# Optimization experiments

Hardware: AMD Instinct MI355X
Metric: run time of the kernel (lower is better)

## Reference

```python
import jax, jax.numpy as jnp
import numpy as np

D_MODEL = 1024
N_HEADS = 16
D_HEAD = D_MODEL // N_HEADS


def setup_inputs() -> dict:
    key = jax.random.key(0)
    ks = jax.random.split(key, 11)
    B, L = 2, 2048
    s = 1.0 / np.sqrt(D_MODEL)
    return {
        "query": jax.random.normal(ks[0], (B, L, D_MODEL), jnp.float32),
        "key": jax.random.normal(ks[1], (B, L, D_MODEL), jnp.float32),
        "value": jax.random.normal(ks[2], (B, L, D_MODEL), jnp.float32),
        "Wq": jax.random.normal(ks[3], (D_MODEL, D_MODEL), jnp.float32) * s,
        "bq": jnp.zeros((D_MODEL,), jnp.float32),
        "Wk": jax.random.normal(ks[4], (D_MODEL, D_MODEL), jnp.float32) * s,
        "bk": jnp.zeros((D_MODEL,), jnp.float32),
        "Wv": jax.random.normal(ks[5], (D_MODEL, D_MODEL), jnp.float32) * s,
        "bv": jnp.zeros((D_MODEL,), jnp.float32),
        "Wo": jax.random.normal(ks[6], (D_MODEL, D_MODEL), jnp.float32) * s,
        "bo": jnp.zeros((D_MODEL,), jnp.float32),
    }


def reference(query, key, value, Wq, bq, Wk, bk, Wv, bv, Wo, bo):
    B, Lq, _ = query.shape
    Lk = key.shape[1]
    scale = D_HEAD ** -0.5
    # projections; weights stored as [in, out] (torch Linear applies x @ W.T; here W is already transposed)
    q = (query @ Wq + bq).reshape(B, Lq, N_HEADS, D_HEAD).transpose(0, 2, 1, 3)  # [B,H,Lq,dh]
    k = (key @ Wk + bk).reshape(B, Lk, N_HEADS, D_HEAD).transpose(0, 2, 1, 3)
    v = (value @ Wv + bv).reshape(B, Lk, N_HEADS, D_HEAD).transpose(0, 2, 1, 3)
    scores = jnp.einsum('bhqd,bhkd->bhqk', q, k) * scale  # [B,H,Lq,Lk]
    # causal mask (is_causal=True)
    causal = jnp.triu(jnp.ones((Lq, Lk), dtype=bool), k=1)
    scores = jnp.where(causal, -jnp.inf, scores)
    attn = jax.nn.softmax(scores, axis=-1)
    out = jnp.einsum('bhqk,bhkd->bhqd', attn, v)  # [B,H,Lq,dh]
    out = out.transpose(0, 2, 1, 3).reshape(B, Lq, D_MODEL)
    return out @ Wo + bo
```

## Files before the change

kernel.cpp:

```cpp
#include <hip/hip_runtime.h>
#include <hip/hip_bf16.h>

typedef __bf16 bf16x8 __attribute__((ext_vector_type(8)));
typedef __bf16 bf16x4 __attribute__((ext_vector_type(4)));
typedef float floatx4 __attribute__((ext_vector_type(4)));

#define MFMA16(a, b, c) __builtin_amdgcn_mfma_f32_16x16x32_bf16(a, b, c, 0, 0, 0)
#define AS1 __attribute__((address_space(1)))
#define AS3 __attribute__((address_space(3)))

constexpr int D = 1024;
constexpr int L = 2048;
constexpr int BB = 2;
constexpr int DH = 64;
constexpr float NEG_BIG = -1e30f;
constexpr float SCALE_LOG2E = 0.125f * 1.4426950408889634f;

__device__ __forceinline__ void gld16(const __bf16* g, __bf16* l) {
  __builtin_amdgcn_global_load_lds((AS1 void*)g, (AS3 void*)l, 16, 0, 0);
}

__global__ __launch_bounds__(256) void cvt_x(const float* __restrict__ xq, const float* __restrict__ xk,
                                             const float* __restrict__ xv, __bf16* __restrict__ out) {
  const int z = blockIdx.z;
  const float* src = z == 0 ? xq : z == 1 ? xk : xv;
  __bf16* dst = out + (size_t)z * BB * L * D;
  const int N = BB * L * D;
  const int stride = gridDim.x * 256 * 4;
  for (int i = (blockIdx.x * 256 + threadIdx.x) * 4; i < N; i += stride) {
    float4 f = *(const float4*)&src[i];
    bf16x4 b = {(__bf16)f.x, (__bf16)f.y, (__bf16)f.z, (__bf16)f.w};
    *(bf16x4*)&dst[i] = b;
  }
}

__global__ void transpose_w(const float* __restrict__ w0, const float* __restrict__ w1,
                            const float* __restrict__ w2, const float* __restrict__ w3,
                            __bf16* __restrict__ out) {
  __shared__ __bf16 tile[32][33];
  int mat = blockIdx.z;
  const float* src = mat == 0 ? w0 : mat == 1 ? w1 : mat == 2 ? w2 : w3;
  __bf16* dst = out + (size_t)mat * D * D;
  int bx = blockIdx.x * 32, by = blockIdx.y * 32;
  int tx = threadIdx.x, ty = threadIdx.y;
#pragma unroll
  for (int i = 0; i < 32; i += 8)
    tile[ty + i][tx] = (__bf16)src[(size_t)(by + ty + i) * D + bx + tx];
  __syncthreads();
#pragma unroll
  for (int i = 0; i < 32; i += 8)
    dst[(size_t)(bx + ty + i) * D + by + tx] = tile[tx][ty + i];
}

__device__ __forceinline__ void gemm_core(const __bf16* __restrict__ A, const __bf16* __restrict__ Bt,
                                          __bf16* sA, __bf16* sB, int m0, int n0,
                                          int wm, int wn, int l15, int quad, int t,
                                          floatx4 (&acc)[4][4]) {
  const int lr = t >> 2;
  const int lc = (t & 3) * 8;
  for (int kb = 0; kb < 1024; kb += 32) {
    gld16(&A[(size_t)(m0 + lr) * 1024 + kb + lc],       &sA[lr * 32 + lc]);
    gld16(&A[(size_t)(m0 + 64 + lr) * 1024 + kb + lc],  &sA[(64 + lr) * 32 + lc]);
    gld16(&Bt[(size_t)(n0 + lr) * 1024 + kb + lc],      &sB[lr * 32 + lc]);
    gld16(&Bt[(size_t)(n0 + 64 + lr) * 1024 + kb + lc], &sB[(64 + lr) * 32 + lc]);
    __syncthreads();

    bf16x8 af[4], bf_[4];
#pragma unroll
    for (int i = 0; i < 4; i++)
      af[i] = *(const bf16x8*)&sA[(wm * 64 + i * 16 + l15) * 32 + quad * 8];
#pragma unroll
    for (int j = 0; j < 4; j++)
      bf_[j] = *(const bf16x8*)&sB[(wn * 64 + j * 16 + l15) * 32 + quad * 8];
#pragma unroll
    for (int i = 0; i < 4; i++)
#pragma unroll
      for (int j = 0; j < 4; j++)
        acc[i][j] = MFMA16(af[i], bf_[j], acc[i][j]);
    __syncthreads();
  }
}

__global__ __launch_bounds__(256) void gemm_proj(const __bf16* __restrict__ xc, const __bf16* __restrict__ wt,
                                                 const float* __restrict__ bq, const float* __restrict__ bk,
                                                 const float* __restrict__ bv, __bf16* __restrict__ qkv) {
  __shared__ __align__(16) __bf16 sA[128 * 32];
  __shared__ __align__(16) __bf16 sB[128 * 32];
  const int z = blockIdx.z;
  const __bf16* A = xc + (size_t)z * BB * L * D;
  const __bf16* Bt = wt + (size_t)z * D * D;
  const float* bias = z == 0 ? bq : z == 1 ? bk : bv;
  __bf16* dst = qkv + (size_t)z * BB * L * D;

  const int t = threadIdx.x;
  const int lane = t & 63;
  const int w = t >> 6;
  const int wm = w >> 1, wn = w & 1;
  const int l15 = lane & 15, quad = lane >> 4;
  const int m0 = blockIdx.y * 128, n0 = blockIdx.x * 128;

  floatx4 acc[4][4];
#pragma unroll
  for (int i = 0; i < 4; i++)
#pragma unroll
    for (int j = 0; j < 4; j++) acc[i][j] = (floatx4){0.f, 0.f, 0.f, 0.f};

  gemm_core(A, Bt, sA, sB, m0, n0, wm, wn, l15, quad, t, acc);

  float bvv[4];
#pragma unroll
  for (int j = 0; j < 4; j++) bvv[j] = bias[n0 + wn * 64 + j * 16 + l15];

#pragma unroll
  for (int i = 0; i < 4; i++) {
    const int rowb = m0 + wm * 64 + i * 16 + quad * 4;
#pragma unroll
    for (int j = 0; j < 4; j++) {
      const int col = n0 + wn * 64 + j * 16 + l15;
      const int h = col >> 6, d = col & 63;
#pragma unroll
      for (int rr = 0; rr < 4; rr++) {
        float val = acc[i][j][rr] + bvv[j];
        const int row = rowb + rr;
        const int b = row >> 11, l = row & 2047;
        if (z == 0) {
          val *= SCALE_LOG2E;
          dst[((size_t)(b * 16 + h) * 2048 + l) * 64 + d] = (__bf16)val;
        } else if (z == 1) {
          dst[((size_t)(b * 16 + h) * 2048 + l) * 64 + d] = (__bf16)val;
        } else {
          dst[((size_t)(b * 16 + h) * 64 + d) * 2048 + l] = (__bf16)val;
        }
      }
    }
  }
}

__global__ __launch_bounds__(256) void gemm_o(const __bf16* __restrict__ ctx, const __bf16* __restrict__ wto,
                                              const float* __restrict__ bo, float* __restrict__ out) {
  __shared__ __align__(16) __bf16 sA[128 * 32];
  __shared__ __align__(16) __bf16 sB[128 * 32];
  const int t = threadIdx.x;
  const int lane = t & 63;
  const int w = t >> 6;
  const int wm = w >> 1, wn = w & 1;
  const int l15 = lane & 15, quad = lane >> 4;
  const int m0 = blockIdx.y * 128, n0 = blockIdx.x * 128;

  floatx4 acc[4][4];
#pragma unroll
  for (int i = 0; i < 4; i++)
#pragma unroll
    for (int j = 0; j < 4; j++) acc[i][j] = (floatx4){0.f, 0.f, 0.f, 0.f};

  gemm_core(ctx, wto, sA, sB, m0, n0, wm, wn, l15, quad, t, acc);

  float bvv[4];
#pragma unroll
  for (int j = 0; j < 4; j++) bvv[j] = bo[n0 + wn * 64 + j * 16 + l15];

#pragma unroll
  for (int i = 0; i < 4; i++) {
    const int rowb = m0 + wm * 64 + i * 16 + quad * 4;
#pragma unroll
    for (int j = 0; j < 4; j++) {
      const int col = n0 + wn * 64 + j * 16 + l15;
#pragma unroll
      for (int rr = 0; rr < 4; rr++)
        out[(size_t)(rowb + rr) * 1024 + col] = acc[i][j][rr] + bvv[j];
    }
  }
}

__global__ __launch_bounds__(256, 4) void flash_attn(const __bf16* __restrict__ q, const __bf16* __restrict__ k,
                                                     const __bf16* __restrict__ vT, __bf16* __restrict__ ctx) {
  __shared__ __align__(16) __bf16 kbuf[2][4096];
  __shared__ __align__(16) __bf16 vbuf[2][4096];

  const int t = threadIdx.x;
  const int lane = t & 63;
  const int w = t >> 6;
  const int l15 = lane & 15, quad = lane >> 4;
  const int bh = blockIdx.y;
  const int qt = (blockIdx.x + blockIdx.y) & 31;
  const int q0 = qt * 64;

  const __bf16* qb = q + (size_t)bh * L * DH;
  const __bf16* kb_ = k + (size_t)bh * L * DH;
  const __bf16* vb = vT + (size_t)bh * DH * L;

  const int qg = q0 + w * 16;
  const int qrow = qg + l15;
  bf16x8 aq0 = *(const bf16x8*)&qb[(size_t)qrow * 64 + quad * 8];
  bf16x8 aq1 = *(const bf16x8*)&qb[(size_t)qrow * 64 + 32 + quad * 8];

  const int c0 = t, c1 = 256 + t;
  const int kr0 = c0 >> 3, kd0 = ((c0 & 7) ^ (kr0 & 7)) * 8;
  const int kr1 = c1 >> 3, kd1 = ((c1 & 7) ^ (kr1 & 7)) * 8;

  floatx4 o[4];
#pragma unroll
  for (int nt = 0; nt < 4; nt++) o[nt] = (floatx4){0.f, 0.f, 0.f, 0.f};
  float psum = 0.f;

  {
    gld16(&kb_[(size_t)kr0 * 64 + kd0], &kbuf[0][c0 * 8]);
    gld16(&kb_[(size_t)kr1 * 64 + kd1], &kbuf[0][c1 * 8]);
    gld16(&vb[(size_t)kr0 * L + kd0],   &vbuf[0][c0 * 8]);
    gld16(&vb[(size_t)kr1 * L + kd1],   &vbuf[0][c1 * 8]);
  }
  __syncthreads();

  for (int it = 0; it <= qt; ++it) {
    const int cur = it & 1;
    const int kt = it * 64;

    if (it < qt) {
      const int ktn = kt + 64;
      gld16(&kb_[(size_t)(ktn + kr0) * 64 + kd0], &kbuf[cur ^ 1][c0 * 8]);
      gld16(&kb_[(size_t)(ktn + kr1) * 64 + kd1], &kbuf[cur ^ 1][c1 * 8]);
      gld16(&vb[(size_t)kr0 * L + ktn + kd0],     &vbuf[cur ^ 1][c0 * 8]);
      gld16(&vb[(size_t)kr1 * L + ktn + kd1],     &vbuf[cur ^ 1][c1 * 8]);
    }

    const bool diag = (it == qt);

#pragma unroll
    for (int sp = 0; sp < 2; ++sp) {
      floatx4 z[2];
#pragma unroll
      for (int u = 0; u < 2; ++u) {
        const int kr = (2 * sp + u) * 16 + l15;
        bf16x8 kf0 = *(const bf16x8*)&kbuf[cur][(kr * 8 + (quad ^ (kr & 7))) * 8];
        bf16x8 kf1 = *(const bf16x8*)&kbuf[cur][(kr * 8 + ((quad + 4) ^ (kr & 7))) * 8];
        floatx4 zz = (floatx4){0.f, 0.f, 0.f, 0.f};
        zz = MFMA16(kf0, aq0, zz);
        zz = MFMA16(kf1, aq1, zz);
        z[u] = zz;
      }

      if (diag) {
#pragma unroll
        for (int u = 0; u < 2; ++u) {
          const int kgb = kt + (2 * sp + u) * 16 + quad * 4;
#pragma unroll
          for (int rr = 0; rr < 4; rr++)
            if (kgb + rr > qrow) z[u][rr] = NEG_BIG;
        }
      }

      bf16x8 pa;
#pragma unroll
      for (int u = 0; u < 2; ++u)
#pragma unroll
        for (int rr = 0; rr < 4; rr++) {
          const float p = __builtin_amdgcn_exp2f(z[u][rr]);
          psum += p;
          pa[u * 4 + rr] = (__bf16)p;
        }

#pragma unroll
      for (int nt = 0; nt < 4; nt++) {
        const int d = nt * 16 + l15;
        const int x0 = (sp * 4 + (quad >> 1)) ^ (d & 7);
        const int x1 = (sp * 4 + 2 + (quad >> 1)) ^ (d & 7);
        union { bf16x8 v8; bf16x4 v4[2]; } uv;
        uv.v4[0] = *(const bf16x4*)&vbuf[cur][(d * 8 + x0) * 8 + (quad & 1) * 4];
        uv.v4[1] = *(const bf16x4*)&vbuf[cur][(d * 8 + x1) * 8 + (quad & 1) * 4];
        o[nt] = MFMA16(pa, uv.v8, o[nt]);
      }
    }
    __syncthreads();
  }

  psum += __shfl_xor(psum, 16);
  psum += __shfl_xor(psum, 32);
  const float invs = 1.f / psum;

  const int b = bh >> 4, h = bh & 15;
#pragma unroll
  for (int rr = 0; rr < 4; rr++) {
    const float inv = __shfl(invs, (lane & 48) + quad * 4 + rr);
    const int row = qg + quad * 4 + rr;
#pragma unroll
    for (int nt = 0; nt < 4; nt++) {
      const int col = h * 64 + nt * 16 + l15;
      ctx[((size_t)b * L + row) * 1024 + col] = (__bf16)(o[nt][rr] * inv);
    }
  }
}

extern "C" void kernel_launch(void* const* d_in, const int* in_sizes, int n_in,
                              void* d_out, int out_size, void* d_ws, size_t ws_size,
                              hipStream_t stream) {
  const float* x_q = (const float*)d_in[0];
  const float* x_k = (const float*)d_in[1];
  const float* x_v = (const float*)d_in[2];
  const float* Wq  = (const float*)d_in[3];
  const float* bq  = (const float*)d_in[4];
  const float* Wk  = (const float*)d_in[5];
  const float* bk  = (const float*)d_in[6];
  const float* Wv  = (const float*)d_in[7];
  const float* bv  = (const float*)d_in[8];
  const float* Wo  = (const float*)d_in[9];
  const float* bo  = (const float*)d_in[10];

  char* ws = (char*)d_ws;
  __bf16* xc  = (__bf16*)ws;
  __bf16* wt  = (__bf16*)(ws + ((size_t)24 << 20));
  __bf16* qkv = (__bf16*)(ws + ((size_t)32 << 20));
  __bf16* ctx = (__bf16*)ws;
  __bf16* qp  = qkv;
  __bf16* kp  = qkv + (size_t)BB * L * D;
  __bf16* vtp = qkv + (size_t)2 * BB * L * D;

  cvt_x<<<dim3(1024, 1, 3), 256, 0, stream>>>(x_q, x_k, x_v, xc);
  transpose_w<<<dim3(32, 32, 4), dim3(32, 8), 0, stream>>>(Wq, Wk, Wv, Wo, wt);
  gemm_proj<<<dim3(8, 32, 3), 256, 0, stream>>>(xc, wt, bq, bk, bv, qkv);
  flash_attn<<<dim3(32, 32), 256, 0, stream>>>(qp, kp, vtp, ctx);
  gemm_o<<<dim3(8, 32), 256, 0, stream>>>(ctx, wt + (size_t)3 * D * D, bo, (float*)d_out);
}
```

Before: 231.2 us.

## Double-buffer LDS tiles in GEMMs and remap block order for XCD locality

The projection and output GEMMs now ping-pong between two LDS buffers, issuing the async global-to-LDS loads for the next K slice before computing on the current one. This removes one barrier per iteration and lets load latency overlap with the MFMAs, at the cost of doubling shared memory per block. Block indices are also remapped so consecutive blocks dispatched round-robin across the 8 XCDs land on neighbouring tiles, which is meant to improve L2 reuse of A and B panels.

```diff
diff --git a/kernel.cpp b/kernel.cpp
--- a/kernel.cpp
+++ b/kernel.cpp
@@ -52,41 +52,60 @@
     dst[(size_t)(bx + ty + i) * D + by + tx] = tile[tx][ty + i];
 }
 
+__device__ __forceinline__ void stage_tile(const __bf16* __restrict__ A, const __bf16* __restrict__ Bt,
+                                           __bf16* sA, __bf16* sB, int m0, int n0, int kb,
+                                           int lr, int lc) {
+  gld16(&A[(size_t)(m0 + lr) * 1024 + kb + lc],       &sA[lr * 32 + lc]);
+  gld16(&A[(size_t)(m0 + 64 + lr) * 1024 + kb + lc],  &sA[(64 + lr) * 32 + lc]);
+  gld16(&Bt[(size_t)(n0 + lr) * 1024 + kb + lc],      &sB[lr * 32 + lc]);
+  gld16(&Bt[(size_t)(n0 + 64 + lr) * 1024 + kb + lc], &sB[(64 + lr) * 32 + lc]);
+}
+
 __device__ __forceinline__ void gemm_core(const __bf16* __restrict__ A, const __bf16* __restrict__ Bt,
-                                          __bf16* sA, __bf16* sB, int m0, int n0,
-                                          int wm, int wn, int l15, int quad, int t,
+                                          __bf16 (&sA)[2][128 * 32], __bf16 (&sB)[2][128 * 32],
+                                          int m0, int n0, int wm, int wn, int l15, int quad, int t,
                                           floatx4 (&acc)[4][4]) {
   const int lr = t >> 2;
   const int lc = (t & 3) * 8;
+
+  stage_tile(A, Bt, sA[0], sB[0], m0, n0, 0, lr, lc);
+  __syncthreads();
+
+  int cur = 0;
   for (int kb = 0; kb < 1024; kb += 32) {
-    gld16(&A[(size_t)(m0 + lr) * 1024 + kb + lc],       &sA[lr * 32 + lc]);
-    gld16(&A[(size_t)(m0 + 64 + lr) * 1024 + kb + lc],  &sA[(64 + lr) * 32 + lc]);
-    gld16(&Bt[(size_t)(n0 + lr) * 1024 + kb + lc],      &sB[lr * 32 + lc]);
-    gld16(&Bt[(size_t)(n0 + 64 + lr) * 1024 + kb + lc], &sB[(64 + lr) * 32 + lc]);
-    __syncthreads();
+    if (kb < 1024 - 32)
+      stage_tile(A, Bt, sA[cur ^ 1], sB[cur ^ 1], m0, n0, kb + 32, lr, lc);
 
     bf16x8 af[4], bf_[4];
 #pragma unroll
     for (int i = 0; i < 4; i++)
-      af[i] = *(const bf16x8*)&sA[(wm * 64 + i * 16 + l15) * 32 + quad * 8];
+      af[i] = *(const bf16x8*)&sA[cur][(wm * 64 + i * 16 + l15) * 32 + quad * 8];
 #pragma unroll
     for (int j = 0; j < 4; j++)
-      bf_[j] = *(const bf16x8*)&sB[(wn * 64 + j * 16 + l15) * 32 + quad * 8];
+      bf_[j] = *(const bf16x8*)&sB[cur][(wn * 64 + j * 16 + l15) * 32 + quad * 8];
 #pragma unroll
     for (int i = 0; i < 4; i++)
 #pragma unroll
       for (int j = 0; j < 4; j++)
         acc[i][j] = MFMA16(af[i], bf_[j], acc[i][j]);
+
     __syncthreads();
+    cur ^= 1;
   }
 }
 
 __global__ __launch_bounds__(256) void gemm_proj(const __bf16* __restrict__ xc, const __bf16* __restrict__ wt,
                                                  const float* __restrict__ bq, const float* __restrict__ bk,
                                                  const float* __restrict__ bv, __bf16* __restrict__ qkv) {
-  __shared__ __align__(16) __bf16 sA[128 * 32];
-  __shared__ __align__(16) __bf16 sB[128 * 32];
-  const int z = blockIdx.z;
+  __shared__ __align__(16) __bf16 sA[2][128 * 32];
+  __shared__ __align__(16) __bf16 sB[2][128 * 32];
+
+  const int flat = (blockIdx.z * 32 + blockIdx.y) * 8 + blockIdx.x;
+  const int s = (flat & 7) * 96 + (flat >> 3);
+  const int z = s >> 8;
+  const int rem = s & 255;
+  const int by = rem >> 3, bx = rem & 7;
+
   const __bf16* A = xc + (size_t)z * BB * L * D;
   const __bf16* Bt = wt + (size_t)z * D * D;
   const float* bias = z == 0 ? bq : z == 1 ? bk : bv;
@@ -97,7 +116,7 @@
   const int w = t >> 6;
   const int wm = w >> 1, wn = w & 1;
   const int l15 = lane & 15, quad = lane >> 4;
-  const int m0 = blockIdx.y * 128, n0 = blockIdx.x * 128;
+  const int m0 = by * 128, n0 = bx * 128;
 
   floatx4 acc[4][4];
 #pragma unroll
@@ -138,14 +157,19 @@
 
 __global__ __launch_bounds__(256) void gemm_o(const __bf16* __restrict__ ctx, const __bf16* __restrict__ wto,
                                               const float* __restrict__ bo, float* __restrict__ out) {
-  __shared__ __align__(16) __bf16 sA[128 * 32];
-  __shared__ __align__(16) __bf16 sB[128 * 32];
+  __shared__ __align__(16) __bf16 sA[2][128 * 32];
+  __shared__ __align__(16) __bf16 sB[2][128 * 32];
+
+  const int flat = blockIdx.y * 8 + blockIdx.x;
+  const int s = (flat & 7) * 32 + (flat >> 3);
+  const int by = s >> 3, bx = s & 7;
+
   const int t = threadIdx.x;
   const int lane = t & 63;
   const int w = t >> 6;
   const int wm = w >> 1, wn = w & 1;
   const int l15 = lane & 15, quad = lane >> 4;
-  const int m0 = blockIdx.y * 128, n0 = blockIdx.x * 128;
+  const int m0 = by * 128, n0 = bx * 128;
 
   floatx4 acc[4][4];
 #pragma unroll
```

Result: no change. 233.0 us (+0.8%).
